# Optimization experiments

Hardware: AMD Instinct MI355X
Metric: run time of the kernel (lower is better)

## Reference

```python
import jax, jax.numpy as jnp
import numpy as np

C, H, O, T, B = 15, 256, 512, 60, 1024


def setup_inputs() -> dict:
    key = jax.random.key(0)
    ks = jax.random.split(key, 8)
    s = 1.0 / np.sqrt(H)
    return {
        "x": jax.random.normal(ks[0], (B, H), dtype=jnp.float32),
        "cam": jax.random.randint(ks[1], (B,), 0, C, dtype=jnp.int32),
        "W_ih": jax.random.uniform(ks[2], (C, 3 * H, H), jnp.float32, -s, s),
        "W_hh": jax.random.uniform(ks[3], (C, 3 * H, H), jnp.float32, -s, s),
        "b_ih": jax.random.uniform(ks[4], (C, 3 * H), jnp.float32, -s, s),
        "b_hh": jax.random.uniform(ks[5], (C, 3 * H), jnp.float32, -s, s),
        "Wc": jax.random.uniform(ks[6], (C, O, H), jnp.float32, -s, s),
        "bc": jax.random.uniform(ks[7], (C, O), jnp.float32, -s, s),
    }


def reference(x, cam, W_ih, W_hh, b_ih, b_hh, Wc, bc):
    # Gather per-sample (per-camera) parameters once.
    Wi = W_ih[cam]          # [B, 3H, H]
    Wh = W_hh[cam]          # [B, 3H, H]
    bi = b_ih[cam]          # [B, 3H]
    bh = b_hh[cam]          # [B, 3H]
    Wcs = Wc[cam]           # [B, O, H]
    bcs = bc[cam]           # [B, O]

    # Input is constant across timesteps -> input gate preactivations computed once.
    gi = jnp.einsum('bh,bgh->bg', x, Wi) + bi   # [B, 3H]
    gi_r, gi_z, gi_n = jnp.split(gi, 3, axis=1)

    h0 = jnp.zeros_like(x)  # [B, H]

    def step(h, _):
        gh = jnp.einsum('bh,bgh->bg', h, Wh) + bh
        gh_r, gh_z, gh_n = jnp.split(gh, 3, axis=1)
        r = jax.nn.sigmoid(gi_r + gh_r)
        z = jax.nn.sigmoid(gi_z + gh_z)
        n = jnp.tanh(gi_n + r * gh_n)
        h_new = (1.0 - z) * n + z * h
        out = jax.nn.sigmoid(jnp.einsum('bh,boh->bo', h_new, Wcs) + bcs)  # [B, O]
        return h_new, out

    _, outs = jax.lax.scan(step, h0, None, length=T)  # [T, B, O]
    return jnp.transpose(outs, (1, 2, 0))             # [B, O, T]
```

## Files before the change

### kernel.cpp

```cpp
#include <hip/hip_runtime.h>
#include <hip/hip_fp16.h>

#define C_    15
#define H_    256
#define O_    512
#define T_    60
#define B_    1024
#define G3H_  768
#define TS    16
#define MAXG  12
#define NSLOT 96
#define NU    80
#define PACKB 300
#define CVTB  2880

typedef __attribute__((ext_vector_type(8))) short bf16x8;
typedef __attribute__((ext_vector_type(4))) float f32x4;

__device__ __forceinline__ unsigned short f2bf(float f) {
    union { float f; unsigned u; } v; v.f = f;
    return (unsigned short)((v.u + 0x7FFFu + ((v.u >> 16) & 1u)) >> 16);
}
__device__ __forceinline__ float sigf(float x) { return 1.f / (1.f + __expf(-x)); }

__global__ __launch_bounds__(256) void prep_kernel(
    const int* __restrict__ cam, const float* __restrict__ Wih,
    const float* __restrict__ Whh, const float* __restrict__ Wc,
    int* __restrict__ order, int* __restrict__ tcam, int* __restrict__ toff,
    int* __restrict__ tcnt, unsigned short* __restrict__ Wih_b,
    unsigned short* __restrict__ Wpack)
{
    int bid = blockIdx.x, tid = threadIdx.x;
    if (bid == 0) {
        __shared__ int cnt[C_], start[C_], fill[C_];
        if (tid < C_) cnt[tid] = 0;
        if (tid < NSLOT) { tcam[tid] = -1; toff[tid] = 0; tcnt[tid] = 0; }
        __syncthreads();
        for (int b = tid; b < B_; b += 256) atomicAdd(&cnt[cam[b]], 1);
        __syncthreads();
        if (tid == 0) {
            int run = 0;
            for (int c = 0; c < C_; ++c) { start[c] = run; fill[c] = run; run += cnt[c]; }
        }
        __syncthreads();
        for (int b = tid; b < B_; b += 256) {
            int pos = atomicAdd(&fill[cam[b]], 1);
            order[pos] = b;
        }
        __syncthreads();
        if (tid == 0) {
            int gcnt[8] = {0,0,0,0,0,0,0,0};
            for (int c = 0; c < C_; ++c) gcnt[c & 7] += (cnt[c] + TS - 1) / TS;
            int maxg = 0;
            for (int g = 0; g < 8; ++g) maxg = max(maxg, gcnt[g]);
            if (maxg <= MAXG) {
                for (int g = 0; g < 8; ++g) {
                    int k = 0;
                    for (int c = g; c < C_; c += 8)
                        for (int r = 0; r < cnt[c]; r += TS) {
                            int slot = g + 8 * k;
                            tcam[slot] = c; toff[slot] = start[c] + r;
                            tcnt[slot] = min(TS, cnt[c] - r); ++k;
                        }
                }
            } else {
                int ti = 0;
                for (int c = 0; c < C_; ++c)
                    for (int r = 0; r < cnt[c]; r += TS) {
                        tcam[ti] = c; toff[ti] = start[c] + r;
                        tcnt[ti] = min(TS, cnt[c] - r); ++ti;
                    }
            }
        }
    } else if (bid <= PACKB) {
        int cu = (bid - 1) * 4 + (tid >> 6);
        int c = cu / NU, u = cu - c * NU;
        int lane = tid & 63, q = lane >> 4, l16 = lane & 15;
        const float* src = (u < 48)
            ? &Whh[((size_t)c * G3H_ + u * 16 + l16) * H_]
            : &Wc[((size_t)c * O_ + (u - 48) * 16 + l16) * H_];
        unsigned short* dst = Wpack + ((size_t)cu * 8) * 512 + lane * 8;
#pragma unroll
        for (int kk = 0; kk < 8; ++kk) {
            float4 v0 = *(const float4*)&src[kk * 32 + q * 8];
            float4 v1 = *(const float4*)&src[kk * 32 + q * 8 + 4];
            unsigned short* d = dst + kk * 512;
            d[0] = f2bf(v0.x); d[1] = f2bf(v0.y); d[2] = f2bf(v0.z); d[3] = f2bf(v0.w);
            d[4] = f2bf(v1.x); d[5] = f2bf(v1.y); d[6] = f2bf(v1.z); d[7] = f2bf(v1.w);
        }
    } else {
        int i = (bid - 1 - PACKB) * 256 + tid;
        float4 v = ((const float4*)Wih)[i];
        unsigned p0 = (unsigned)f2bf(v.x) | ((unsigned)f2bf(v.y) << 16);
        unsigned p1 = (unsigned)f2bf(v.z) | ((unsigned)f2bf(v.w) << 16);
        ((uint2*)Wih_b)[i] = make_uint2(p0, p1);
    }
}

__global__ __launch_bounds__(384) void gi_mfma(
    const float* __restrict__ x, const unsigned short* __restrict__ Wih_b,
    const float* __restrict__ bih, const float* __restrict__ bhh,
    const int* __restrict__ order, const int* __restrict__ tcam,
    const int* __restrict__ toff, const int* __restrict__ tcnt,
    float* __restrict__ gi)
{
    int c = tcam[blockIdx.x]; if (c < 0) return;
    int cnt = tcnt[blockIdx.x], off = toff[blockIdx.x];
    int tid = threadIdx.x;
    __shared__ unsigned short hbfs[TS * 264];
    for (int idx = tid; idx < TS * 64; idx += 384) {
        int m = idx >> 6, c4 = idx & 63;
        float4 v = make_float4(0.f, 0.f, 0.f, 0.f);
        if (m < cnt) v = *(const float4*)&x[(size_t)order[off + m] * H_ + (c4 << 2)];
        unsigned p0 = (unsigned)f2bf(v.x) | ((unsigned)f2bf(v.y) << 16);
        unsigned p1 = (unsigned)f2bf(v.z) | ((unsigned)f2bf(v.w) << 16);
        *(uint2*)&hbfs[m * 264 + (c4 << 2)] = make_uint2(p0, p1);
    }
    __syncthreads();
    int w = tid >> 6, lane = tid & 63, q = lane >> 4, l16 = lane & 15;
    f32x4 acc[2][4];
#pragma unroll
    for (int i = 0; i < 2; ++i)
#pragma unroll
        for (int nt = 0; nt < 4; ++nt) acc[i][nt] = (f32x4){0.f, 0.f, 0.f, 0.f};
    const unsigned short* bp[2];
#pragma unroll
    for (int i = 0; i < 2; ++i)
        bp[i] = Wih_b + ((size_t)c * G3H_ + (2 * w + i) * 64 + l16) * H_;
    const unsigned short* ap = &hbfs[l16 * 264 + q * 8];
#pragma unroll 2
    for (int kk = 0; kk < 8; ++kk) {
        bf16x8 a = *(const bf16x8*)(ap + kk * 32);
#pragma unroll
        for (int i = 0; i < 2; ++i)
#pragma unroll
            for (int nt = 0; nt < 4; ++nt) {
                bf16x8 b = *(const bf16x8*)(bp[i] + (size_t)nt * 16 * H_ + kk * 32 + q * 8);
                acc[i][nt] = __builtin_amdgcn_mfma_f32_16x16x32_bf16(a, b, acc[i][nt], 0, 0, 0);
            }
    }
#pragma unroll
    for (int i = 0; i < 2; ++i) {
        int u = 2 * w + i;
#pragma unroll
        for (int nt = 0; nt < 4; ++nt) {
            int col = u * 64 + nt * 16 + l16;
            float bias = bih[c * G3H_ + col] + (col < 2 * H_ ? bhh[c * G3H_ + col] : 0.f);
#pragma unroll
            for (int r = 0; r < 4; ++r) {
                int m = q * 4 + r;
                gi[((size_t)(blockIdx.x * TS + m)) * G3H_ + col] = acc[i][nt][r] + bias;
            }
        }
    }
}

__global__ __launch_bounds__(512, 1) void persist_kernel(
    const unsigned short* __restrict__ Wpack, const float* __restrict__ bhh,
    const float* __restrict__ gi, const int* __restrict__ tcam,
    unsigned short* __restrict__ htraj)
{
    int slot = blockIdx.x;
    int c = tcam[slot]; if (c < 0) return;
    int tid = threadIdx.x, w = tid >> 6, lane = tid & 63, q = lane >> 4, l16 = lane & 15;

    __shared__ unsigned short hbf[2][16][264];

    bf16x8 wf[6][8];
#pragma unroll
    for (int ii = 0; ii < 3; ++ii)
#pragma unroll
        for (int jj = 0; jj < 2; ++jj)
#pragma unroll
            for (int kk = 0; kk < 8; ++kk)
                wf[ii * 2 + jj][kk] = *(const bf16x8*)(
                    Wpack + (((size_t)(c * NU + ii * 16 + w + 8 * jj)) * 8 + kk) * 512 + lane * 8);

    float gir[2][4], giz[2][4], gin[2][4], bhn[2], hreg[2][4];
#pragma unroll
    for (int i = 0; i < 2; ++i) {
        int col = (w + 8 * i) * 16 + l16;
        bhn[i] = bhh[c * G3H_ + 2 * H_ + col];
#pragma unroll
        for (int r = 0; r < 4; ++r) {
            size_t row = (size_t)(slot * TS + q * 4 + r) * G3H_;
            gir[i][r] = gi[row + col];
            giz[i][r] = gi[row + H_ + col];
            gin[i][r] = gi[row + 2 * H_ + col];
            hreg[i][r] = 0.f;
        }
    }
    unsigned short* hp = htraj + ((size_t)slot * TS + q * 4) * 256 + w * 16 + l16;

#pragma unroll 2
    for (int s = 0; s < T_; ++s) {
        int wbuf = s & 1, rbuf = wbuf ^ 1;
        f32x4 acc[6];
#pragma unroll
        for (int i = 0; i < 2; ++i)
#pragma unroll
            for (int r = 0; r < 4; ++r) {
                acc[i][r] = gir[i][r];
                acc[2 + i][r] = giz[i][r];
                acc[4 + i][r] = bhn[i];
            }
        if (s > 0) {
#pragma unroll
            for (int kk = 0; kk < 8; ++kk) {
                bf16x8 a = *(const bf16x8*)&hbf[rbuf][l16][kk * 32 + q * 8];
#pragma unroll
                for (int ui = 0; ui < 6; ++ui)
                    acc[ui] = __builtin_amdgcn_mfma_f32_16x16x32_bf16(a, wf[ui][kk], acc[ui], 0, 0, 0);
            }
        }
#pragma unroll
        for (int i = 0; i < 2; ++i) {
            int col = (w + 8 * i) * 16 + l16;
#pragma unroll
            for (int r = 0; r < 4; ++r) {
                float rr = sigf(acc[i][r]);
                float zz = sigf(acc[2 + i][r]);
                float pre = gin[i][r] + rr * acc[4 + i][r];
                float nn = 2.f * sigf(2.f * pre) - 1.f;
                float hn = (1.f - zz) * nn + zz * hreg[i][r];
                hreg[i][r] = hn;
                unsigned short hb = f2bf(hn);
                hbf[wbuf][q * 4 + r][col] = hb;
                hp[r * 256 + i * 128] = hb;
            }
        }
        hp += (size_t)NSLOT * TS * 256;
        asm volatile("s_waitcnt lgkmcnt(0)" ::: "memory");
        __builtin_amdgcn_s_barrier();
        __builtin_amdgcn_sched_barrier(0);
    }
}

__global__ __launch_bounds__(512, 2) void out_kernel(
    const unsigned short* __restrict__ Wpack, const float* __restrict__ bc,
    const unsigned short* __restrict__ htraj, const int* __restrict__ order,
    const int* __restrict__ tcam, const int* __restrict__ toff,
    const int* __restrict__ tcnt, float* __restrict__ outp)
{
    int slot = blockIdx.x;
    int c = tcam[slot]; if (c < 0) return;
    int n = tcnt[slot], off = toff[slot];
    int tz = blockIdx.z;
    int tid = threadIdx.x, w = tid >> 6, lane = tid & 63, q = lane >> 4, l16 = lane & 15;
    __shared__ unsigned short hb[2][16][264];
    __shared__ int ord16[16];
    if (tid < 16) ord16[tid] = (tid < n) ? order[off + tid] : -1;

    int u = blockIdx.y * 8 + w;
    bf16x8 wf[8];
    const unsigned short* wb = Wpack + ((size_t)c * NU + 48 + u) * 8 * 512 + lane * 8;
#pragma unroll
    for (int kk = 0; kk < 8; ++kk) wf[kk] = *(const bf16x8*)(wb + (size_t)kk * 512);
    float bcr = bc[c * O_ + u * 16 + l16];

    int m = tid >> 5, c8 = (tid & 31) * 8;
    const unsigned short* hsrc =
        &htraj[(((size_t)(tz * 10) * NSLOT + slot) * 16 + m) * 256 + c8];
    uint4 stg = *(const uint4*)hsrc;
    *(uint4*)&hb[0][m][c8] = stg;
    __syncthreads();

    float vals[4][10];
#pragma unroll
    for (int ti = 0; ti < 10; ++ti) {
        int cur = ti & 1;
        if (ti + 1 < 10)
            stg = *(const uint4*)(hsrc + (size_t)(ti + 1) * NSLOT * TS * 256);
        f32x4 acc = (f32x4){0.f, 0.f, 0.f, 0.f};
#pragma unroll
        for (int kk = 0; kk < 8; ++kk) {
            bf16x8 a = *(const bf16x8*)&hb[cur][l16][kk * 32 + q * 8];
            acc = __builtin_amdgcn_mfma_f32_16x16x32_bf16(a, wf[kk], acc, 0, 0, 0);
        }
#pragma unroll
        for (int r = 0; r < 4; ++r) vals[r][ti] = sigf(acc[r] + bcr);
        if (ti + 1 < 10) {
            *(uint4*)&hb[cur ^ 1][m][c8] = stg;
            asm volatile("s_waitcnt lgkmcnt(0)" ::: "memory");
            __builtin_amdgcn_s_barrier();
            __builtin_amdgcn_sched_barrier(0);
        }
    }
    int o = u * 16 + l16;
#pragma unroll
    for (int r = 0; r < 4; ++r) {
        int b = ord16[q * 4 + r];
        if (b >= 0) {
            float* dst = &outp[((size_t)b * O_ + o) * T_ + tz * 10];
#pragma unroll
            for (int j = 0; j < 5; ++j)
                *(float2*)&dst[j * 2] = make_float2(vals[r][2 * j], vals[r][2 * j + 1]);
        }
    }
}

extern "C" void kernel_launch(void* const* d_in, const int* in_sizes, int n_in,
                              void* d_out, int out_size, void* d_ws, size_t ws_size,
                              hipStream_t stream)
{
    const float* x   = (const float*)d_in[0];
    const int*   cam = (const int*)d_in[1];
    const float* Wih = (const float*)d_in[2];
    const float* Whh = (const float*)d_in[3];
    const float* bih = (const float*)d_in[4];
    const float* bhh = (const float*)d_in[5];
    const float* Wc  = (const float*)d_in[6];
    const float* bc  = (const float*)d_in[7];
    float* outp = (float*)d_out;

    char* w = (char*)d_ws;
    unsigned short* Wih_b = (unsigned short*)w; w += (size_t)C_ * G3H_ * H_ * 2;
    unsigned short* Wpack = (unsigned short*)w; w += (size_t)C_ * NU * 8 * 512 * 2;
    int* order = (int*)w; w += B_ * 4;
    int* tcam  = (int*)w; w += NSLOT * 4;
    int* toff  = (int*)w; w += NSLOT * 4;
    int* tcnt  = (int*)w; w += NSLOT * 4;
    float* gi  = (float*)w; w += (size_t)NSLOT * TS * G3H_ * 4;
    unsigned short* htraj = (unsigned short*)w;

    prep_kernel<<<1 + PACKB + CVTB, 256, 0, stream>>>(cam, Wih, Whh, Wc, order, tcam,
                                                      toff, tcnt, Wih_b, Wpack);
    gi_mfma<<<NSLOT, 384, 0, stream>>>(x, Wih_b, bih, bhh, order, tcam, toff, tcnt, gi);
    persist_kernel<<<NSLOT, 512, 0, stream>>>(Wpack, bhh, gi, tcam, htraj);
    out_kernel<<<dim3(NSLOT, 4, 6), 512, 0, stream>>>(Wpack, bc, htraj, order, tcam,
                                                      toff, tcnt, outp);
}
```

Measured before the change: 491.5 us.

## Fuse input-gate GEMM into persistent GRU kernel via shared-memory staging

Removes the separate gi_mfma launch and instead computes the input-gate preactivations at the start of the persistent recurrence kernel. The results go into a transposed shared-memory buffer rather than a global gi array. Each timestep then reads the r/z/n input terms from LDS instead of holding them in registers, and the b_hh n-bias is added explicitly. This saves a kernel launch and a global round trip, and frees registers; launch bounds change to allow 2 blocks per CU. The cost is about 61KB of LDS plus extra LDS reads in the serial loop.

Result: faster. 434.1 us (-11.7%).

```diff
diff --git a/kernel.cpp b/kernel.cpp
--- a/kernel.cpp
+++ b/kernel.cpp
@@ -97,74 +97,54 @@
     }
 }
 
-__global__ __launch_bounds__(384) void gi_mfma(
+__global__ __launch_bounds__(512, 2) void persist_kernel(
     const float* __restrict__ x, const unsigned short* __restrict__ Wih_b,
-    const float* __restrict__ bih, const float* __restrict__ bhh,
-    const int* __restrict__ order, const int* __restrict__ tcam,
-    const int* __restrict__ toff, const int* __restrict__ tcnt,
-    float* __restrict__ gi)
+    const unsigned short* __restrict__ Wpack, const float* __restrict__ bih,
+    const float* __restrict__ bhh, const int* __restrict__ order,
+    const int* __restrict__ tcam, const int* __restrict__ toff,
+    const int* __restrict__ tcnt, unsigned short* __restrict__ htraj)
 {
-    int c = tcam[blockIdx.x]; if (c < 0) return;
-    int cnt = tcnt[blockIdx.x], off = toff[blockIdx.x];
-    int tid = threadIdx.x;
-    __shared__ unsigned short hbfs[TS * 264];
-    for (int idx = tid; idx < TS * 64; idx += 384) {
+    int slot = blockIdx.x;
+    int c = tcam[slot]; if (c < 0) return;
+    int cnt = tcnt[slot], off = toff[slot];
+    int tid = threadIdx.x, w = tid >> 6, lane = tid & 63, q = lane >> 4, l16 = lane & 15;
+
+    __shared__ float gisT[G3H_][20];
+    __shared__ unsigned short hbf[2][16][264];
+
+    for (int idx = tid; idx < TS * 64; idx += 512) {
         int m = idx >> 6, c4 = idx & 63;
         float4 v = make_float4(0.f, 0.f, 0.f, 0.f);
         if (m < cnt) v = *(const float4*)&x[(size_t)order[off + m] * H_ + (c4 << 2)];
         unsigned p0 = (unsigned)f2bf(v.x) | ((unsigned)f2bf(v.y) << 16);
         unsigned p1 = (unsigned)f2bf(v.z) | ((unsigned)f2bf(v.w) << 16);
-        *(uint2*)&hbfs[m * 264 + (c4 << 2)] = make_uint2(p0, p1);
+        *(uint2*)&hbf[0][m][c4 << 2] = make_uint2(p0, p1);
     }
     __syncthreads();
-    int w = tid >> 6, lane = tid & 63, q = lane >> 4, l16 = lane & 15;
-    f32x4 acc[2][4];
-#pragma unroll
-    for (int i = 0; i < 2; ++i)
-#pragma unroll
-        for (int nt = 0; nt < 4; ++nt) acc[i][nt] = (f32x4){0.f, 0.f, 0.f, 0.f};
-    const unsigned short* bp[2];
-#pragma unroll
-    for (int i = 0; i < 2; ++i)
-        bp[i] = Wih_b + ((size_t)c * G3H_ + (2 * w + i) * 64 + l16) * H_;
-    const unsigned short* ap = &hbfs[l16 * 264 + q * 8];
-#pragma unroll 2
-    for (int kk = 0; kk < 8; ++kk) {
-        bf16x8 a = *(const bf16x8*)(ap + kk * 32);
-#pragma unroll
-        for (int i = 0; i < 2; ++i)
-#pragma unroll
-            for (int nt = 0; nt < 4; ++nt) {
-                bf16x8 b = *(const bf16x8*)(bp[i] + (size_t)nt * 16 * H_ + kk * 32 + q * 8);
-                acc[i][nt] = __builtin_amdgcn_mfma_f32_16x16x32_bf16(a, b, acc[i][nt], 0, 0, 0);
+
+    {
+        f32x4 acc[6];
+#pragma unroll
+        for (int ui = 0; ui < 6; ++ui) acc[ui] = (f32x4){0.f, 0.f, 0.f, 0.f};
+#pragma unroll
+        for (int kk = 0; kk < 8; ++kk) {
+            bf16x8 a = *(const bf16x8*)&hbf[0][l16][kk * 32 + q * 8];
+#pragma unroll
+            for (int ui = 0; ui < 6; ++ui) {
+                int col = (w * 6 + ui) * 16 + l16;
+                bf16x8 b = *(const bf16x8*)(Wih_b + ((size_t)c * G3H_ + col) * H_ + kk * 32 + q * 8);
+                acc[ui] = __builtin_amdgcn_mfma_f32_16x16x32_bf16(a, b, acc[ui], 0, 0, 0);
             }
-    }
-#pragma unroll
-    for (int i = 0; i < 2; ++i) {
-        int u = 2 * w + i;
-#pragma unroll
-        for (int nt = 0; nt < 4; ++nt) {
-            int col = u * 64 + nt * 16 + l16;
+        }
+#pragma unroll
+        for (int ui = 0; ui < 6; ++ui) {
+            int col = (w * 6 + ui) * 16 + l16;
             float bias = bih[c * G3H_ + col] + (col < 2 * H_ ? bhh[c * G3H_ + col] : 0.f);
 #pragma unroll
-            for (int r = 0; r < 4; ++r) {
-                int m = q * 4 + r;
-                gi[((size_t)(blockIdx.x * TS + m)) * G3H_ + col] = acc[i][nt][r] + bias;
-            }
-        }
-    }
-}
-
-__global__ __launch_bounds__(512, 1) void persist_kernel(
-    const unsigned short* __restrict__ Wpack, const float* __restrict__ bhh,
-    const float* __restrict__ gi, const int* __restrict__ tcam,
-    unsigned short* __restrict__ htraj)
-{
-    int slot = blockIdx.x;
-    int c = tcam[slot]; if (c < 0) return;
-    int tid = threadIdx.x, w = tid >> 6, lane = tid & 63, q = lane >> 4, l16 = lane & 15;
-
-    __shared__ unsigned short hbf[2][16][264];
+            for (int r = 0; r < 4; ++r) gisT[col][q * 4 + r] = acc[ui][r] + bias;
+        }
+    }
+    __builtin_amdgcn_sched_barrier(0);
 
     bf16x8 wf[6][8];
 #pragma unroll
@@ -176,34 +156,23 @@
                 wf[ii * 2 + jj][kk] = *(const bf16x8*)(
                     Wpack + (((size_t)(c * NU + ii * 16 + w + 8 * jj)) * 8 + kk) * 512 + lane * 8);
 
-    float gir[2][4], giz[2][4], gin[2][4], bhn[2], hreg[2][4];
+    float bhn[2], hreg[2][4];
 #pragma unroll
     for (int i = 0; i < 2; ++i) {
         int col = (w + 8 * i) * 16 + l16;
         bhn[i] = bhh[c * G3H_ + 2 * H_ + col];
 #pragma unroll
-        for (int r = 0; r < 4; ++r) {
-            size_t row = (size_t)(slot * TS + q * 4 + r) * G3H_;
-            gir[i][r] = gi[row + col];
-            giz[i][r] = gi[row + H_ + col];
-            gin[i][r] = gi[row + 2 * H_ + col];
-            hreg[i][r] = 0.f;
-        }
+        for (int r = 0; r < 4; ++r) hreg[i][r] = 0.f;
     }
     unsigned short* hp = htraj + ((size_t)slot * TS + q * 4) * 256 + w * 16 + l16;
+    __syncthreads();
 
 #pragma unroll 2
     for (int s = 0; s < T_; ++s) {
         int wbuf = s & 1, rbuf = wbuf ^ 1;
         f32x4 acc[6];
 #pragma unroll
-        for (int i = 0; i < 2; ++i)
-#pragma unroll
-            for (int r = 0; r < 4; ++r) {
-                acc[i][r] = gir[i][r];
-                acc[2 + i][r] = giz[i][r];
-                acc[4 + i][r] = bhn[i];
-            }
+        for (int ui = 0; ui < 6; ++ui) acc[ui] = (f32x4){0.f, 0.f, 0.f, 0.f};
         if (s > 0) {
 #pragma unroll
             for (int kk = 0; kk < 8; ++kk) {
@@ -216,11 +185,14 @@
 #pragma unroll
         for (int i = 0; i < 2; ++i) {
             int col = (w + 8 * i) * 16 + l16;
+            f32x4 gr = *(const f32x4*)&gisT[col][q * 4];
+            f32x4 gz = *(const f32x4*)&gisT[H_ + col][q * 4];
+            f32x4 gn = *(const f32x4*)&gisT[2 * H_ + col][q * 4];
 #pragma unroll
             for (int r = 0; r < 4; ++r) {
-                float rr = sigf(acc[i][r]);
-                float zz = sigf(acc[2 + i][r]);
-                float pre = gin[i][r] + rr * acc[4 + i][r];
+                float rr = sigf(gr[r] + acc[i][r]);
+                float zz = sigf(gz[r] + acc[2 + i][r]);
+                float pre = gn[r] + rr * (acc[4 + i][r] + bhn[i]);
                 float nn = 2.f * sigf(2.f * pre) - 1.f;
                 float hn = (1.f - zz) * nn + zz * hreg[i][r];
                 hreg[i][r] = hn;
@@ -320,13 +292,12 @@
     int* tcam  = (int*)w; w += NSLOT * 4;
     int* toff  = (int*)w; w += NSLOT * 4;
     int* tcnt  = (int*)w; w += NSLOT * 4;
-    float* gi  = (float*)w; w += (size_t)NSLOT * TS * G3H_ * 4;
     unsigned short* htraj = (unsigned short*)w;
 
     prep_kernel<<<1 + PACKB + CVTB, 256, 0, stream>>>(cam, Wih, Whh, Wc, order, tcam,
                                                       toff, tcnt, Wih_b, Wpack);
-    gi_mfma<<<NSLOT, 384, 0, stream>>>(x, Wih_b, bih, bhh, order, tcam, toff, tcnt, gi);
-    persist_kernel<<<NSLOT, 512, 0, stream>>>(Wpack, bhh, gi, tcam, htraj);
+    persist_kernel<<<NSLOT, 512, 0, stream>>>(x, Wih_b, Wpack, bih, bhh, order, tcam,
+                                              toff, tcnt, htraj);
     out_kernel<<<dim3(NSLOT, 4, 6), 512, 0, stream>>>(Wpack, bc, htraj, order, tcam,
                                                       toff, tcnt, outp);
 }
```
